# Performance work log

Measured on AMD Instinct MI355X. Metric: run time of the kernel, lower is better.

## Reference

```python
import jax, jax.numpy as jnp
import numpy as np

IN_FEATURES = 512
OUT_FEATURES = 128
KERNEL_DIM = 32
BATCH = 128


def setup_inputs() -> dict:
    key = jax.random.key(0)
    kx, kT = jax.random.split(key)
    x = jax.random.normal(kx, (BATCH, IN_FEATURES), dtype=jnp.float32)
    # nn.Parameter initialized with normal(0, 1)
    T = jax.random.normal(kT, (IN_FEATURES, OUT_FEATURES, KERNEL_DIM), dtype=jnp.float32)
    return {"x": x, "T": T}


def reference(x, T):
    B = x.shape[0]
    in_f, out_f, k_dim = T.shape
    # projection: [B, in] @ [in, out*k] -> [B, out, k]
    m = (x @ T.reshape(in_f, out_f * k_dim)).reshape(B, out_f, k_dim)
    # pairwise L1 distance over kernel dim: [B, B, out]
    # original: M = m[None], M_T = m[:, None]; norm = |M - M_T|.sum(3); o_b = exp(-norm).sum(0) - 1
    norm = jnp.abs(m[None, :, :, :] - m[:, None, :, :]).sum(axis=-1)  # [i=B, j=B, out]
    o_b = jnp.exp(-norm).sum(axis=0) - 1.0  # [B, out] (subtract self-distance term exp(0)=1)
    return jnp.concatenate([x, o_b], axis=1)  # [B, in + out]
```

## Files before the change

### kernel.cpp

```cpp
#include <hip/hip_runtime.h>
#include <hip/hip_fp16.h>

#define IN_F    512
#define NC      4096
#define OUT_COLS 640
#define B_SZ    128
#define MOH_PITCH 72

typedef __attribute__((ext_vector_type(8)))  short bf16x8;
typedef __attribute__((ext_vector_type(16))) float f32x16;

union H2x4  { uint4 u4; __half2 h[4]; };
union FragB { unsigned int u[4]; bf16x8 s; };

static __device__ __forceinline__ unsigned int pack2(float lo, float hi) {
    return (__float_as_uint(lo) >> 16) | (__float_as_uint(hi) & 0xFFFF0000u);
}
static __device__ __forceinline__ __half2 habs2_(__half2 v) {
    unsigned int u = *(unsigned int*)&v & 0x7FFF7FFFu;
    return *(__half2*)&u;
}

__global__ __launch_bounds__(256) void prep_kernel(
    const float* __restrict__ x, float* __restrict__ out,
    unsigned short* __restrict__ xa)
{
    const int g = blockIdx.x * 256 + threadIdx.x;
    const int b = g >> 7, c4 = g & 127;
    float4 v = ((const float4*)x)[g];
    *(float4*)(out + b * OUT_COLS + c4 * 4) = v;
    const int slot = ((b >> 5) * 32 + (c4 >> 2)) * 64 + ((c4 >> 1) & 1) * 32 + (b & 31);
    uint2 pv; pv.x = pack2(v.x, v.y); pv.y = pack2(v.z, v.w);
    *(uint2*)(xa + (size_t)slot * 8 + (c4 & 1) * 4) = pv;
}

__global__ __launch_bounds__(1024) void fused_kernel(
    const unsigned short* __restrict__ xa,
    const float* __restrict__ T,
    float* __restrict__ out)
{
    __shared__ __align__(16) char smem[65536];
    float*  red  = (float*)smem;
    __half* moh  = (__half*)smem;
    float*  psum = (float*)(smem + 18432);

    const int tid    = threadIdx.x;
    const int lane   = tid & 63;
    const int w      = tid >> 6;
    const int o      = blockIdx.x & 127;
    const int jhalf  = blockIdx.x >> 7;
    const int mt     = w & 3;
    const int kg     = w >> 2;
    const int col    = lane & 31;
    const int half32 = lane >> 5;

    f32x16 acc = {0.f,0.f,0.f,0.f,0.f,0.f,0.f,0.f,0.f,0.f,0.f,0.f,0.f,0.f,0.f,0.f};
    const unsigned short* pa = xa + ((size_t)(mt * 32 + kg * 8) * 64 + lane) * 8;
    const float* pb = T + (size_t)(kg * 128 + half32 * 8) * NC + o * 32 + col;
    #pragma unroll
    for (int ch = 0; ch < 8; ++ch) {
        bf16x8 af = *(const bf16x8*)(pa + (size_t)ch * 512);
        const float* tb = pb + (size_t)ch * 16 * NC;
        float b0 = tb[0*NC], b1 = tb[1*NC], b2 = tb[2*NC], b3 = tb[3*NC];
        float b4 = tb[4*NC], b5 = tb[5*NC], b6 = tb[6*NC], b7 = tb[7*NC];
        FragB bf;
        bf.u[0] = pack2(b0, b1); bf.u[1] = pack2(b2, b3);
        bf.u[2] = pack2(b4, b5); bf.u[3] = pack2(b6, b7);
        acc = __builtin_amdgcn_mfma_f32_32x32x16_bf16(af, bf.s, acc, 0, 0, 0);
    }
    {
        float* rd = red + kg * 4096 + mt * 1024 + col;
        #pragma unroll
        for (int r = 0; r < 16; ++r) {
            int row = (r & 3) + 8 * (r >> 2) + 4 * half32;
            rd[row * 32] = acc[r];
        }
    }
    __syncthreads();

    float4 s;
    {
        const int e = tid * 4;
        s = *(const float4*)&red[e];
        #pragma unroll
        for (int p = 1; p < 4; ++p) {
            float4 v2 = *(const float4*)&red[p * 4096 + e];
            s.x += v2.x; s.y += v2.y; s.z += v2.z; s.w += v2.w;
        }
    }
    __syncthreads();
    {
        const int e = tid * 4;
        const int mtt = e >> 10, row = (e >> 5) & 31, c0 = e & 31;
        __half2 lo = __floats2half2_rn(s.x, s.y);
        __half2 hi = __floats2half2_rn(s.z, s.w);
        uint2 w2; w2.x = *(unsigned int*)&lo; w2.y = *(unsigned int*)&hi;
        *(uint2*)&moh[(mtt * 32 + row) * MOH_PITCH + c0] = w2;
    }
    __syncthreads();

    const int jj5 = tid & 31;
    const int isl = tid >> 5;
    const int j0  = jhalf * 64 + jj5;

    __half2 mj0[16], mj1[16];
    #pragma unroll
    for (int k16 = 0; k16 < 4; ++k16) {
        H2x4 a, b;
        a.u4 = *(const uint4*)&moh[j0 * MOH_PITCH + k16 * 8];
        b.u4 = *(const uint4*)&moh[(j0 + 32) * MOH_PITCH + k16 * 8];
        #pragma unroll
        for (int h = 0; h < 4; ++h) { mj0[k16*4+h] = a.h[h]; mj1[k16*4+h] = b.h[h]; }
    }

    float s0 = 0.f, s1 = 0.f;
    #pragma unroll
    for (int ii = 0; ii < 4; ++ii) {
        const int i = isl * 4 + ii;
        __half2 n0 = __float2half2_rn(0.f), n1 = __float2half2_rn(0.f);
        #pragma unroll
        for (int k16 = 0; k16 < 4; ++k16) {
            H2x4 mi; mi.u4 = *(const uint4*)&moh[i * MOH_PITCH + k16 * 8];
            #pragma unroll
            for (int h = 0; h < 4; ++h) {
                n0 = __hadd2(n0, habs2_(__hsub2(mj0[k16*4+h], mi.h[h])));
                n1 = __hadd2(n1, habs2_(__hsub2(mj1[k16*4+h], mi.h[h])));
            }
        }
        float2 f0 = __half22float2(n0), f1 = __half22float2(n1);
        s0 += __expf(-(f0.x + f0.y));
        s1 += __expf(-(f1.x + f1.y));
    }
    psum[jj5 * 33 + isl]        = s0;
    psum[1056 + jj5 * 33 + isl] = s1;
    __syncthreads();
    if (tid < 64) {
        int jsel = tid >> 5, jj = tid & 31;
        float tot = 0.f;
        #pragma unroll
        for (int u = 0; u < 32; ++u) tot += psum[jsel * 1056 + jj * 33 + u];
        out[(jhalf * 64 + jsel * 32 + jj) * OUT_COLS + IN_F + o] = tot - 1.0f;
    }
}

extern "C" void kernel_launch(void* const* d_in, const int* in_sizes, int n_in,
                              void* d_out, int out_size, void* d_ws, size_t ws_size,
                              hipStream_t stream) {
    const float* x = (const float*)d_in[0];
    const float* T = (const float*)d_in[1];
    float* out = (float*)d_out;
    unsigned short* xa = (unsigned short*)d_ws;

    prep_kernel<<<64, 256, 0, stream>>>(x, out, xa);
    fused_kernel<<<256, 1024, 0, stream>>>(xa, T, out);
}
```

Measured before the change: 69.94 us.

## Split fused kernel into 512 blocks of 512 threads with quarter-j partitioning

Cuts the fused kernel from 1024 to 512 threads per block. Each wave now covers twice the K range (16 MFMA steps instead of 8), so only two partial reductions remain in shared memory. The grid doubles to 512 blocks, and each block handles a quarter of the j rows instead of half. This raises the block count and the chance of co-residency on the CUs, and it shrinks the shared-memory footprint. In exchange, each block recomputes the full projection, so the duplicated GEMM and T reads go from 2x to 4x per output column.

```diff
diff --git a/kernel.cpp b/kernel.cpp
--- a/kernel.cpp
+++ b/kernel.cpp
@@ -4,7 +4,6 @@
 #define IN_F    512
 #define NC      4096
 #define OUT_COLS 640
-#define B_SZ    128
 #define MOH_PITCH 72
 
 typedef __attribute__((ext_vector_type(8)))  short bf16x8;
@@ -34,31 +33,30 @@
     *(uint2*)(xa + (size_t)slot * 8 + (c4 & 1) * 4) = pv;
 }
 
-__global__ __launch_bounds__(1024) void fused_kernel(
+__global__ __launch_bounds__(512, 4) void fused_kernel(
     const unsigned short* __restrict__ xa,
     const float* __restrict__ T,
     float* __restrict__ out)
 {
-    __shared__ __align__(16) char smem[65536];
-    float*  red  = (float*)smem;
-    __half* moh  = (__half*)smem;
-    float*  psum = (float*)(smem + 18432);
+    __shared__ float red[2 * 4096];
+    __shared__ __align__(16) __half moh[128 * MOH_PITCH];
+    __shared__ float psum[2 * 528];
 
     const int tid    = threadIdx.x;
     const int lane   = tid & 63;
     const int w      = tid >> 6;
     const int o      = blockIdx.x & 127;
-    const int jhalf  = blockIdx.x >> 7;
+    const int jq     = blockIdx.x >> 7;
     const int mt     = w & 3;
     const int kg     = w >> 2;
     const int col    = lane & 31;
     const int half32 = lane >> 5;
 
     f32x16 acc = {0.f,0.f,0.f,0.f,0.f,0.f,0.f,0.f,0.f,0.f,0.f,0.f,0.f,0.f,0.f,0.f};
-    const unsigned short* pa = xa + ((size_t)(mt * 32 + kg * 8) * 64 + lane) * 8;
-    const float* pb = T + (size_t)(kg * 128 + half32 * 8) * NC + o * 32 + col;
+    const unsigned short* pa = xa + ((size_t)(mt * 32 + kg * 16) * 64 + lane) * 8;
+    const float* pb = T + (size_t)(kg * 256 + half32 * 8) * NC + o * 32 + col;
     #pragma unroll
-    for (int ch = 0; ch < 8; ++ch) {
+    for (int ch = 0; ch < 16; ++ch) {
         bf16x8 af = *(const bf16x8*)(pa + (size_t)ch * 512);
         const float* tb = pb + (size_t)ch * 16 * NC;
         float b0 = tb[0*NC], b1 = tb[1*NC], b2 = tb[2*NC], b3 = tb[3*NC];
@@ -78,37 +76,36 @@
     }
     __syncthreads();
 
-    float4 s;
     {
-        const int e = tid * 4;
-        s = *(const float4*)&red[e];
-        #pragma unroll
-        for (int p = 1; p < 4; ++p) {
-            float4 v2 = *(const float4*)&red[p * 4096 + e];
-            s.x += v2.x; s.y += v2.y; s.z += v2.z; s.w += v2.w;
-        }
-    }
-    __syncthreads();
-    {
-        const int e = tid * 4;
-        const int mtt = e >> 10, row = (e >> 5) & 31, c0 = e & 31;
-        __half2 lo = __floats2half2_rn(s.x, s.y);
-        __half2 hi = __floats2half2_rn(s.z, s.w);
-        uint2 w2; w2.x = *(unsigned int*)&lo; w2.y = *(unsigned int*)&hi;
-        *(uint2*)&moh[(mtt * 32 + row) * MOH_PITCH + c0] = w2;
+        const int e0 = tid * 4, e1 = 2048 + tid * 4;
+        float4 a0 = *(const float4*)&red[e0];
+        float4 p0 = *(const float4*)&red[4096 + e0];
+        float4 a1 = *(const float4*)&red[e1];
+        float4 p1 = *(const float4*)&red[4096 + e1];
+        a0.x += p0.x; a0.y += p0.y; a0.z += p0.z; a0.w += p0.w;
+        a1.x += p1.x; a1.y += p1.y; a1.z += p1.z; a1.w += p1.w;
+        const int m0t = e0 >> 10, r0 = (e0 >> 5) & 31, c0 = e0 & 31;
+        const int m1t = e1 >> 10, r1 = (e1 >> 5) & 31, c1 = e1 & 31;
+        __half2 l0 = __floats2half2_rn(a0.x, a0.y), h0 = __floats2half2_rn(a0.z, a0.w);
+        __half2 l1 = __floats2half2_rn(a1.x, a1.y), h1 = __floats2half2_rn(a1.z, a1.w);
+        uint2 w0, w1;
+        w0.x = *(unsigned int*)&l0; w0.y = *(unsigned int*)&h0;
+        w1.x = *(unsigned int*)&l1; w1.y = *(unsigned int*)&h1;
+        *(uint2*)&moh[(m0t * 32 + r0) * MOH_PITCH + c0] = w0;
+        *(uint2*)&moh[(m1t * 32 + r1) * MOH_PITCH + c1] = w1;
     }
     __syncthreads();
 
-    const int jj5 = tid & 31;
-    const int isl = tid >> 5;
-    const int j0  = jhalf * 64 + jj5;
+    const int jj4 = tid & 15;
+    const int isl = tid >> 4;
+    const int j0  = jq * 32 + jj4;
 
     __half2 mj0[16], mj1[16];
     #pragma unroll
     for (int k16 = 0; k16 < 4; ++k16) {
         H2x4 a, b;
         a.u4 = *(const uint4*)&moh[j0 * MOH_PITCH + k16 * 8];
-        b.u4 = *(const uint4*)&moh[(j0 + 32) * MOH_PITCH + k16 * 8];
+        b.u4 = *(const uint4*)&moh[(j0 + 16) * MOH_PITCH + k16 * 8];
         #pragma unroll
         for (int h = 0; h < 4; ++h) { mj0[k16*4+h] = a.h[h]; mj1[k16*4+h] = b.h[h]; }
     }
@@ -131,15 +128,15 @@
         s0 += __expf(-(f0.x + f0.y));
         s1 += __expf(-(f1.x + f1.y));
     }
-    psum[jj5 * 33 + isl]        = s0;
-    psum[1056 + jj5 * 33 + isl] = s1;
+    psum[jj4 * 33 + isl]       = s0;
+    psum[528 + jj4 * 33 + isl] = s1;
     __syncthreads();
-    if (tid < 64) {
-        int jsel = tid >> 5, jj = tid & 31;
+    if (tid < 32) {
+        int jsel = tid >> 4, jj = tid & 15;
         float tot = 0.f;
         #pragma unroll
-        for (int u = 0; u < 32; ++u) tot += psum[jsel * 1056 + jj * 33 + u];
-        out[(jhalf * 64 + jsel * 32 + jj) * OUT_COLS + IN_F + o] = tot - 1.0f;
+        for (int u = 0; u < 32; ++u) tot += psum[jsel * 528 + jj * 33 + u];
+        out[(jq * 32 + jsel * 16 + jj) * OUT_COLS + IN_F + o] = tot - 1.0f;
     }
 }
 
@@ -152,5 +149,5 @@
     unsigned short* xa = (unsigned short*)d_ws;
 
     prep_kernel<<<64, 256, 0, stream>>>(x, out, xa);
-    fused_kernel<<<256, 1024, 0, stream>>>(xa, T, out);
+    fused_kernel<<<512, 512, 0, stream>>>(xa, T, out);
 }
```

Result: slower. 72.30 us (+3.4%).
